# Kernel optimization log

Hardware: AMD Instinct MI355X
Metric: run time of the kernel (lower is better)

## Reference

```python
import jax, jax.numpy as jnp
import numpy as np

HIDDEN = 1024
HEADS = 16
HEAD_DIM = HIDDEN // HEADS


def setup_inputs() -> dict:
    key = jax.random.key(0)
    k_x, k_wq, k_bq, k_wo, k_bo = jax.random.split(key, 5)
    x = jax.random.normal(k_x, (2, 2048, HIDDEN), dtype=jnp.float32)
    s = 1.0 / np.sqrt(HIDDEN)
    W_qkv = jax.random.uniform(k_wq, (HIDDEN, 3 * HIDDEN), jnp.float32, -s, s)
    b_qkv = jax.random.uniform(k_bq, (3 * HIDDEN,), jnp.float32, -s, s)
    W_out = jax.random.uniform(k_wo, (HIDDEN, HIDDEN), jnp.float32, -s, s)
    b_out = jax.random.uniform(k_bo, (HIDDEN,), jnp.float32, -s, s)
    return {"x": x, "W_qkv": W_qkv, "b_qkv": b_qkv, "W_out": W_out, "b_out": b_out}


def reference(x, W_qkv, b_qkv, W_out, b_out):
    B, S, D = x.shape
    qkv = x @ W_qkv + b_qkv                       # [B,S,3D]
    qkv = qkv.reshape(B, S, 3, HEADS, HEAD_DIM)
    qkv = jnp.transpose(qkv, (2, 0, 3, 1, 4))     # [3,B,H,S,Dh]
    q, k, v = qkv[0], qkv[1], qkv[2]
    scores = jnp.einsum("bhsd,bhtd->bhst", q, k) / np.sqrt(HEAD_DIM)
    attn = jax.nn.softmax(scores, axis=-1)        # [B,H,S,S]
    out = jnp.einsum("bhst,bhtd->bhsd", attn, v)  # [B,H,S,Dh]
    out = jnp.transpose(out, (0, 2, 1, 3)).reshape(B, S, D)
    return out @ W_out + b_out
```

## Files before the change

kernel.cpp:

```cpp
#include <hip/hip_runtime.h>
#include <hip/hip_bf16.h>

typedef short short8 __attribute__((ext_vector_type(8)));
typedef float float4_ __attribute__((ext_vector_type(4)));
typedef unsigned short ushort_t;
typedef unsigned int uint32_t_;
typedef uint32_t_ uint2v __attribute__((ext_vector_type(2)));
typedef uint32_t_ uint4v __attribute__((ext_vector_type(4)));

#define SCL 0.1803368801111f

__device__ __forceinline__ ushort_t f2bf(float f) {
    uint32_t_ u = __builtin_bit_cast(uint32_t_, f);
    u = (u + 0x7fffu + ((u >> 16) & 1u)) >> 16;
    return (ushort_t)u;
}

__device__ __forceinline__ uint32_t_ pack_bf16(float a, float b) {
    uint32_t_ ua = __builtin_bit_cast(uint32_t_, a) + 0x8000u;
    uint32_t_ ub = __builtin_bit_cast(uint32_t_, b) + 0x8000u;
    return __builtin_amdgcn_perm(ub, ua, 0x07060302);
}

__device__ __forceinline__ uint32_t_ cvt_pk_bf16(float lo, float hi) {
    uint32_t_ r;
    asm("v_cvt_pk_bf16_f32 %0, %1, %2" : "=v"(r) : "v"(lo), "v"(hi));
    return r;
}

#define MFMA32(a, b, c) __builtin_amdgcn_mfma_f32_16x16x32_bf16(a, b, c, 0, 0, 0)

#define GLD_LDS16(g, l) __builtin_amdgcn_global_load_lds( \
    (const __attribute__((address_space(1))) void*)(g),   \
    (__attribute__((address_space(3))) void*)(l), 16, 0, 0)

__global__ __launch_bounds__(256)
void prep_k(const float* __restrict__ x, ushort_t* __restrict__ x_bf,
            const float* __restrict__ Wqkv, ushort_t* __restrict__ WqkvT,
            const float* __restrict__ Wout, ushort_t* __restrict__ WoutT) {
    __shared__ float tile[32][33];
    const int id = blockIdx.x;
    const int tid = threadIdx.x;
    if (id < 4096) {
        int i = (id * 256 + tid) * 4;
        float4 v = *(const float4*)(x + i);
        uint32_t_ lo = (uint32_t_)f2bf(v.x) | ((uint32_t_)f2bf(v.y) << 16);
        uint32_t_ hi = (uint32_t_)f2bf(v.z) | ((uint32_t_)f2bf(v.w) << 16);
        *(uint2*)(x_bf + i) = make_uint2(lo, hi);
        return;
    }
    const float* in;
    ushort_t* out;
    int N, K, n0, k0;
    if (id < 7168) {
        int t = id - 4096;
        in = Wqkv; out = WqkvT; N = 3072; K = 1024;
        n0 = (t % 96) * 32; k0 = (t / 96) * 32;
    } else {
        int t = id - 7168;
        in = Wout; out = WoutT; N = 1024; K = 1024;
        n0 = (t & 31) * 32; k0 = (t >> 5) * 32;
    }
    int tx = tid & 31, ty = tid >> 5;
    #pragma unroll
    for (int i = 0; i < 32; i += 8)
        tile[ty + i][tx] = in[(size_t)(k0 + ty + i) * N + n0 + tx];
    __syncthreads();
    #pragma unroll
    for (int i = 0; i < 32; i += 8)
        out[(size_t)(n0 + ty + i) * K + k0 + tx] = f2bf(tile[tx][ty + i]);
}

template <int TN, bool QKV_EPI>
__global__ __launch_bounds__(256, TN == 128 ? 3 : 4)
void gemm_dbuf_k(const ushort_t* __restrict__ A, const ushort_t* __restrict__ Bt,
                 const float* __restrict__ bias, void* __restrict__ C,
                 ushort_t* __restrict__ Vt_out, int M, int N, int K) {
    constexpr int NB   = TN / 32;
    constexpr int SETB = 8192 + TN * 64;
    __shared__ char smem[2 * SETB];
    const int tid  = threadIdx.x;
    const int m0   = blockIdx.y * 128;
    const int n0   = blockIdx.x * TN;
    const int w    = tid >> 6;
    const int lane = tid & 63;
    const int wm   = (w >> 1) * 64;
    const int wn   = (w & 1) * (TN / 2);
    const int quad = lane >> 4;
    const int l16  = lane & 15;

    const int sr = 16 * w + (lane >> 2);
    const int sc = ((lane & 3) ^ ((sr >> 1) & 3)) * 8;
    const ushort_t* ag0 = A  + (size_t)(m0 + sr) * K + sc;
    const ushort_t* ag1 = A  + (size_t)(m0 + sr + 64) * K + sc;
    const ushort_t* bg0 = Bt + (size_t)(n0 + sr) * K + sc;
    const ushort_t* bg1 = Bt + (size_t)(n0 + sr + 64) * K + sc;
    char* sA = smem + 1024 * w;
    char* sB = smem + 8192 + 1024 * w;

    int aoff[4], boff[NB];
    #pragma unroll
    for (int i = 0; i < 4; i++) {
        int row = wm + i * 16 + l16;
        aoff[i] = row * 64 + ((quad ^ ((row >> 1) & 3)) * 16);
    }
    #pragma unroll
    for (int i = 0; i < NB; i++) {
        int row = wn + i * 16 + l16;
        boff[i] = 8192 + row * 64 + ((quad ^ ((row >> 1) & 3)) * 16);
    }

    float4_ acc[4][NB] = {};
    const int NIT = K >> 5;

    GLD_LDS16(ag0, sA);
    GLD_LDS16(ag1, sA + 4096);
    GLD_LDS16(bg0, sB);
    if (TN == 128) GLD_LDS16(bg1, sB + 4096);

    for (int it = 0; it < NIT; ++it) {
        __syncthreads();
        if (it + 1 < NIT) {
            const int nk = (it + 1) * 32;
            char* dA = sA + ((it + 1) & 1) * SETB;
            char* dB = sB + ((it + 1) & 1) * SETB;
            GLD_LDS16(ag0 + nk, dA);
            GLD_LDS16(ag1 + nk, dA + 4096);
            GLD_LDS16(bg0 + nk, dB);
            if (TN == 128) GLD_LDS16(bg1 + nk, dB + 4096);
        }
        const char* base = smem + (it & 1) * SETB;
        short8 af[4], bf[NB];
        #pragma unroll
        for (int i = 0; i < 4; i++)  af[i] = *(const short8*)(base + aoff[i]);
        #pragma unroll
        for (int i = 0; i < NB; i++) bf[i] = *(const short8*)(base + boff[i]);
        #pragma unroll
        for (int mi = 0; mi < 4; mi++)
            #pragma unroll
            for (int ni = 0; ni < NB; ni++)
                acc[mi][ni] = MFMA32(af[mi], bf[ni], acc[mi][ni]);
    }

    #pragma unroll
    for (int mi = 0; mi < 4; mi++) {
        int row = m0 + wm + mi * 16 + quad * 4;
        #pragma unroll
        for (int ni = 0; ni < NB; ni++) {
            int col = n0 + wn + ni * 16 + l16;
            float bb = bias[col];
            if (QKV_EPI) {
                if (col < 2048) {
                    float sc2 = (col < 1024) ? SCL : 1.0f;
                    #pragma unroll
                    for (int r = 0; r < 4; r++)
                        ((ushort_t*)C)[(size_t)(row + r) * 2048 + col] =
                            f2bf((acc[mi][ni][r] + bb) * sc2);
                } else {
                    int s0v  = row & 2047;
                    int spos = (s0v & ~31) | (quad << 3) | ((mi & 1) << 2);
                    size_t vrow = (size_t)((row >> 11) * 1024 + (col - 2048));
                    float v0 = acc[mi][ni][0] + bb, v1 = acc[mi][ni][1] + bb;
                    float v2 = acc[mi][ni][2] + bb, v3 = acc[mi][ni][3] + bb;
                    uint2v pk;
                    pk.x = pack_bf16(v0, v1);
                    pk.y = pack_bf16(v2, v3);
                    *(uint2v*)(Vt_out + vrow * 2048 + spos) = pk;
                }
            } else {
                #pragma unroll
                for (int r = 0; r < 4; r++)
                    ((float*)C)[(size_t)(row + r) * N + col] = acc[mi][ni][r] + bb;
            }
        }
    }
}

__global__ __launch_bounds__(256, 5)
void flash_attn_k(const ushort_t* __restrict__ qk, const ushort_t* __restrict__ vt,
                  ushort_t* __restrict__ out) {
    __shared__ char smem[32768];
    const int bh = blockIdx.x;
    const int b  = bh >> 4, h = bh & 15;
    const int q0 = blockIdx.y * 64;
    const int tid  = threadIdx.x;
    const int w    = tid >> 6;
    const int lane = tid & 63;
    const int quad = lane >> 4;
    const int l16  = lane & 15;
    const int qh   = w >> 1;
    const int kh   = w & 1;
    const size_t tok0 = (size_t)b * 2048;
    const int hq = h * 64;

    const int r0 = 16 * w + (lane >> 3), r1 = r0 + 8;
    const int s7 = lane & 7;
    const int c0 = (s7 ^ ((r0 >> 1) & 7)) * 8;
    const int c1 = (s7 ^ ((r1 >> 1) & 7)) * 8;
    const ushort_t* qg0 = qk + (tok0 + q0 + r0) * 2048 + hq + c0;
    const ushort_t* qg1 = qk + (tok0 + q0 + r1) * 2048 + hq + c1;
    const ushort_t* kg0 = qk + (tok0 + r0) * 2048 + 1024 + hq + c0;
    const ushort_t* kg1 = qk + (tok0 + r1) * 2048 + 1024 + hq + c1;
    const ushort_t* vg0 = vt + (size_t)(bh * 64 + r0) * 2048 + c0;
    const ushort_t* vg1 = vt + (size_t)(bh * 64 + r1) * 2048 + c1;
    char* stK = smem + 2048 * w;
    char* stV = smem + 8192 + 2048 * w;
    char* stQ = smem + 16384 + 2048 * w;

    GLD_LDS16(qg0, stQ);
    GLD_LDS16(qg1, stQ + 1024);
    GLD_LDS16(kg0, stK);
    GLD_LDS16(kg1, stK + 1024);
    GLD_LDS16(vg0, stV);
    GLD_LDS16(vg1, stV + 1024);
    __syncthreads();

    const int sw = (l16 >> 1) & 7;
    short8 qf[2][2];
    #pragma unroll
    for (int sub = 0; sub < 2; sub++)
        #pragma unroll
        for (int kk = 0; kk < 2; kk++) {
            int row = qh * 32 + sub * 16 + l16;
            qf[sub][kk] = *(const short8*)(smem + 16384 + row * 128 +
                                           (((kk * 4 + quad) ^ sw) * 16));
        }

    int koff[2][2], voff[4];
    #pragma unroll
    for (int mi = 0; mi < 2; mi++)
        #pragma unroll
        for (int kk = 0; kk < 2; kk++) {
            int row = kh * 32 + mi * 16 + l16;
            koff[mi][kk] = row * 128 + (((kk * 4 + quad) ^ sw) * 16);
        }
    #pragma unroll
    for (int di = 0; di < 4; di++) {
        int row = di * 16 + l16;
        voff[di] = 8192 + row * 128 + (((kh * 4 + quad) ^ sw) * 16);
    }

    float4_ ot[2][4] = {};
    float lsum[2] = {0.f, 0.f};

    for (int kt = 0; kt < 2048; kt += 64) {
        __syncthreads();
        const int set = (kt >> 6) & 1;
        if (kt + 64 < 2048) {
            const int nb = (set ^ 1) * 16384;
            const size_t go = (size_t)(kt + 64);
            GLD_LDS16(kg0 + go * 2048, stK + nb);
            GLD_LDS16(kg1 + go * 2048, stK + nb + 1024);
            GLD_LDS16(vg0 + go, stV + nb);
            GLD_LDS16(vg1 + go, stV + nb + 1024);
        }
        const char* base = smem + set * 16384;

        float4_ st[2][2];
        #pragma unroll
        for (int mi = 0; mi < 2; mi++) {
            short8 kf0 = *(const short8*)(base + koff[mi][0]);
            short8 kf1 = *(const short8*)(base + koff[mi][1]);
            #pragma unroll
            for (int sub = 0; sub < 2; sub++) {
                float4_ z = {0.f, 0.f, 0.f, 0.f};
                z = MFMA32(kf0, qf[sub][0], z);
                z = MFMA32(kf1, qf[sub][1], z);
                st[mi][sub] = z;
            }
        }

        short8 bp32[2];
        #pragma unroll
        for (int sub = 0; sub < 2; sub++) {
            uint4v u;
            #pragma unroll
            for (int mi = 0; mi < 2; mi++) {
                float p0 = __builtin_amdgcn_exp2f(st[mi][sub][0]);
                float p1 = __builtin_amdgcn_exp2f(st[mi][sub][1]);
                float p2 = __builtin_amdgcn_exp2f(st[mi][sub][2]);
                float p3 = __builtin_amdgcn_exp2f(st[mi][sub][3]);
                lsum[sub] += (p0 + p1) + (p2 + p3);
                if (mi == 0) { u.x = cvt_pk_bf16(p0, p1); u.y = cvt_pk_bf16(p2, p3); }
                else         { u.z = cvt_pk_bf16(p0, p1); u.w = cvt_pk_bf16(p2, p3); }
            }
            bp32[sub] = __builtin_bit_cast(short8, u);
        }

        #pragma unroll
        for (int di = 0; di < 4; di++) {
            short8 vv = *(const short8*)(base + voff[di]);
            #pragma unroll
            for (int sub = 0; sub < 2; sub++)
                ot[sub][di] = MFMA32(vv, bp32[sub], ot[sub][di]);
        }
    }

    #pragma unroll
    for (int sub = 0; sub < 2; sub++) {
        float t = lsum[sub];
        t += __shfl_xor(t, 16, 64);
        t += __shfl_xor(t, 32, 64);
        lsum[sub] = t;
    }

    float* Obuf = (float*)smem;
    float* lbuf = (float*)(smem + 17408);
    __syncthreads();
    #pragma unroll
    for (int sub = 0; sub < 2; sub++)
        lbuf[(qh * 32 + sub * 16 + l16) * 2 + kh] = lsum[sub];
    if (kh == 1) {
        #pragma unroll
        for (int sub = 0; sub < 2; sub++)
            #pragma unroll
            for (int di = 0; di < 4; di++)
                *(float4_*)&Obuf[(qh * 32 + sub * 16 + l16) * 68 + di * 16 + quad * 4] = ot[sub][di];
    }
    __syncthreads();
    if (kh == 0) {
        #pragma unroll
        for (int sub = 0; sub < 2; sub++)
            #pragma unroll
            for (int di = 0; di < 4; di++) {
                float4_* p = (float4_*)&Obuf[(qh * 32 + sub * 16 + l16) * 68 + di * 16 + quad * 4];
                *p = *p + ot[sub][di];
            }
    }
    __syncthreads();

    {
        int q  = tid >> 2;
        int ds = (tid & 3) * 16;
        float linv = 1.0f / (lbuf[q * 2] + lbuf[q * 2 + 1]);
        const float* ob = &Obuf[q * 68 + ds];
        float4_ v0 = *(const float4_*)(ob);
        float4_ v1 = *(const float4_*)(ob + 4);
        float4_ v2 = *(const float4_*)(ob + 8);
        float4_ v3 = *(const float4_*)(ob + 12);
        uint4v d0, d1;
        d0.x = pack_bf16(v0[0] * linv, v0[1] * linv);
        d0.y = pack_bf16(v0[2] * linv, v0[3] * linv);
        d0.z = pack_bf16(v1[0] * linv, v1[1] * linv);
        d0.w = pack_bf16(v1[2] * linv, v1[3] * linv);
        d1.x = pack_bf16(v2[0] * linv, v2[1] * linv);
        d1.y = pack_bf16(v2[2] * linv, v2[3] * linv);
        d1.z = pack_bf16(v3[0] * linv, v3[1] * linv);
        d1.w = pack_bf16(v3[2] * linv, v3[3] * linv);
        ushort_t* dst = out + (tok0 + q0 + (size_t)q) * 1024 + hq + ds;
        *(uint4v*)(dst)     = d0;
        *(uint4v*)(dst + 8) = d1;
    }
}

extern "C" void kernel_launch(void* const* d_in, const int* in_sizes, int n_in,
                              void* d_out, int out_size, void* d_ws, size_t ws_size,
                              hipStream_t stream) {
    const float* x    = (const float*)d_in[0];
    const float* Wqkv = (const float*)d_in[1];
    const float* bqkv = (const float*)d_in[2];
    const float* Wout = (const float*)d_in[3];
    const float* bout = (const float*)d_in[4];
    float* out = (float*)d_out;

    char* ws = (char*)d_ws;
    ushort_t* x_bf    = (ushort_t*)(ws);
    ushort_t* WqkvT   = (ushort_t*)(ws + 8388608);
    ushort_t* WoutT   = (ushort_t*)(ws + 14680064);
    ushort_t* qk_bf   = (ushort_t*)(ws + 16777216);
    ushort_t* vt_bf   = (ushort_t*)(ws + 33554432);
    ushort_t* attn_bf = (ushort_t*)(ws + 41943040);

    prep_k<<<8192, 256, 0, stream>>>(x, x_bf, Wqkv, WqkvT, Wout, WoutT);

    gemm_dbuf_k<128, true><<<dim3(24, 32), 256, 0, stream>>>(
        x_bf, WqkvT, bqkv, (void*)qk_bf, vt_bf, 4096, 3072, 1024);

    flash_attn_k<<<dim3(32, 32), 256, 0, stream>>>(qk_bf, vt_bf, attn_bf);

    gemm_dbuf_k<64, false><<<dim3(16, 32), 256, 0, stream>>>(
        attn_bf, WoutT, bout, (void*)out, nullptr, 4096, 1024, 1024);
}
```

Before: 178.3 us.

## Software-pipeline flash attention PV MFMAs one tile behind QK and softmax

Peels the first K/V tile and restructures the attention loop so the P·V MFMAs for the previous tile run while the current tile's QK scores and exp2 are computed. V fragments and packed probabilities are carried across iterations in registers, which lets MFMA and transcendental work overlap. Launch bounds drop from 5 to 4 waves per SIMD to make room for the extra live registers, at the cost of some occupancy.

```diff
diff --git a/kernel.cpp b/kernel.cpp
--- a/kernel.cpp
+++ b/kernel.cpp
@@ -176,7 +176,7 @@
     }
 }
 
-__global__ __launch_bounds__(256, 5)
+__global__ __launch_bounds__(256, 4)
 void flash_attn_k(const ushort_t* __restrict__ qk, const ushort_t* __restrict__ vt,
                   ushort_t* __restrict__ out) {
     __shared__ char smem[32768];
@@ -242,8 +242,50 @@
 
     float4_ ot[2][4] = {};
     float lsum[2] = {0.f, 0.f};
-
-    for (int kt = 0; kt < 2048; kt += 64) {
+    short8 vprev[4];
+    short8 bpprev[2];
+
+    {
+        __syncthreads();
+        GLD_LDS16(kg0 + (size_t)64 * 2048, stK + 16384);
+        GLD_LDS16(kg1 + (size_t)64 * 2048, stK + 16384 + 1024);
+        GLD_LDS16(vg0 + 64, stV + 16384);
+        GLD_LDS16(vg1 + 64, stV + 16384 + 1024);
+        const char* base = smem;
+        float4_ st[2][2];
+        #pragma unroll
+        for (int mi = 0; mi < 2; mi++) {
+            short8 kf0 = *(const short8*)(base + koff[mi][0]);
+            short8 kf1 = *(const short8*)(base + koff[mi][1]);
+            #pragma unroll
+            for (int sub = 0; sub < 2; sub++) {
+                float4_ z = {0.f, 0.f, 0.f, 0.f};
+                z = MFMA32(kf0, qf[sub][0], z);
+                z = MFMA32(kf1, qf[sub][1], z);
+                st[mi][sub] = z;
+            }
+        }
+        #pragma unroll
+        for (int di = 0; di < 4; di++)
+            vprev[di] = *(const short8*)(base + voff[di]);
+        #pragma unroll
+        for (int sub = 0; sub < 2; sub++) {
+            uint4v u;
+            #pragma unroll
+            for (int mi = 0; mi < 2; mi++) {
+                float p0 = __builtin_amdgcn_exp2f(st[mi][sub][0]);
+                float p1 = __builtin_amdgcn_exp2f(st[mi][sub][1]);
+                float p2 = __builtin_amdgcn_exp2f(st[mi][sub][2]);
+                float p3 = __builtin_amdgcn_exp2f(st[mi][sub][3]);
+                lsum[sub] += (p0 + p1) + (p2 + p3);
+                if (mi == 0) { u.x = cvt_pk_bf16(p0, p1); u.y = cvt_pk_bf16(p2, p3); }
+                else         { u.z = cvt_pk_bf16(p0, p1); u.w = cvt_pk_bf16(p2, p3); }
+            }
+            bpprev[sub] = __builtin_bit_cast(short8, u);
+        }
+    }
+
+    for (int kt = 64; kt < 2048; kt += 64) {
         __syncthreads();
         const int set = (kt >> 6) & 1;
         if (kt + 64 < 2048) {
@@ -270,7 +312,16 @@
             }
         }
 
-        short8 bp32[2];
+        #pragma unroll
+        for (int di = 0; di < 4; di++)
+            #pragma unroll
+            for (int sub = 0; sub < 2; sub++)
+                ot[sub][di] = MFMA32(vprev[di], bpprev[sub], ot[sub][di]);
+
+        #pragma unroll
+        for (int di = 0; di < 4; di++)
+            vprev[di] = *(const short8*)(base + voff[di]);
+
         #pragma unroll
         for (int sub = 0; sub < 2; sub++) {
             uint4v u;
@@ -284,17 +335,15 @@
                 if (mi == 0) { u.x = cvt_pk_bf16(p0, p1); u.y = cvt_pk_bf16(p2, p3); }
                 else         { u.z = cvt_pk_bf16(p0, p1); u.w = cvt_pk_bf16(p2, p3); }
             }
-            bp32[sub] = __builtin_bit_cast(short8, u);
-        }
-
-        #pragma unroll
-        for (int di = 0; di < 4; di++) {
-            short8 vv = *(const short8*)(base + voff[di]);
-            #pragma unroll
-            for (int sub = 0; sub < 2; sub++)
-                ot[sub][di] = MFMA32(vv, bp32[sub], ot[sub][di]);
-        }
-    }
+            bpprev[sub] = __builtin_bit_cast(short8, u);
+        }
+    }
+
+    #pragma unroll
+    for (int di = 0; di < 4; di++)
+        #pragma unroll
+        for (int sub = 0; sub < 2; sub++)
+            ot[sub][di] = MFMA32(vprev[di], bpprev[sub], ot[sub][di]);
 
     #pragma unroll
     for (int sub = 0; sub < 2; sub++) {
```

Result: no change. 176.3 us (-1.1%).
